# Kernel tuning notes

Measured on AMD Instinct MI355X. Metric: run time of the kernel, lower is better.

## Reference

```python
import jax, jax.numpy as jnp
import numpy as np

NUM_HEADS = 8

def setup_inputs() -> dict:
    key = jax.random.key(0)
    ks = jax.random.split(key, 7)
    B, S, H = 2, 4096, 512
    sc = 1.0 / np.sqrt(H)
    x = jax.random.normal(ks[0], (B, S, H), dtype=jnp.float32)
    Wq = jax.random.normal(ks[1], (H, H), dtype=jnp.float32) * sc
    bq = jnp.zeros((H,), dtype=jnp.float32)
    Wk = jax.random.normal(ks[2], (H, H), dtype=jnp.float32) * sc
    bk = jnp.zeros((H,), dtype=jnp.float32)
    Wv = jax.random.normal(ks[3], (H, H), dtype=jnp.float32) * sc
    bv = jnp.zeros((H,), dtype=jnp.float32)
    return {"x": x, "Wq": Wq, "bq": bq, "Wk": Wk, "bk": bk, "Wv": Wv, "bv": bv}

def reference(x, Wq, bq, Wk, bk, Wv, bv):
    B, S, H = x.shape
    hd = H // NUM_HEADS
    def split_heads(t):  # [B,S,H] -> [B,nh,S,hd]
        return t.reshape(B, S, NUM_HEADS, hd).transpose(0, 2, 1, 3)
    q = split_heads(x @ Wq + bq)
    k = split_heads(x @ Wk + bk)
    v = split_heads(x @ Wv + bv)
    scores = jnp.einsum('bhqd,bhkd->bhqk', q, k) / jnp.sqrt(jnp.float32(hd))
    attn = jax.nn.softmax(scores, axis=-1)  # dropout is identity at inference
    out = jnp.einsum('bhqk,bhkd->bhqd', attn, v)
    return out.transpose(0, 2, 1, 3).reshape(B, S, H)
```

## Files before the change

### kernel.cpp

```cpp
#include <hip/hip_runtime.h>
#include <hip/hip_bf16.h>

typedef __attribute__((ext_vector_type(8))) short short8;
typedef __attribute__((ext_vector_type(4))) float float4v;
typedef __attribute__((ext_vector_type(16))) float f32x16;

using bf16 = __hip_bfloat16;

#define QSCALE 0.18033688011112042f

__device__ inline float fexp2(float x) { return __builtin_amdgcn_exp2f(x); }

__device__ inline short f2bf(float f) {
  __hip_bfloat16 h = __float2bfloat16(f);
  short s;
  __builtin_memcpy(&s, &h, 2);
  return s;
}

__device__ inline float4v mfma16(short8 a, short8 b, float4v c) {
  return __builtin_amdgcn_mfma_f32_16x16x32_bf16(a, b, c, 0, 0, 0);
}
__device__ inline f32x16 mfma32(short8 a, short8 b, f32x16 c) {
  return __builtin_amdgcn_mfma_f32_32x32x16_bf16(a, b, c, 0, 0, 0);
}
__device__ inline unsigned pk2(float lo, float hi) {
  __hip_bfloat16 l = __float2bfloat16(lo), h = __float2bfloat16(hi);
  unsigned short ls, hs;
  __builtin_memcpy(&ls, &l, 2);
  __builtin_memcpy(&hs, &h, 2);
  return (unsigned)ls | ((unsigned)hs << 16);
}


__global__ __launch_bounds__(256) void conv_x_kernel(const float* __restrict__ x,
                                                     bf16* __restrict__ xb) {
  int i = blockIdx.x * 256 + threadIdx.x;
  const float4v* src = reinterpret_cast<const float4v*>(x);
  float4v a = src[(size_t)i * 2];
  float4v c = src[(size_t)i * 2 + 1];
  short8 o;
  o[0] = f2bf(a[0]); o[1] = f2bf(a[1]); o[2] = f2bf(a[2]); o[3] = f2bf(a[3]);
  o[4] = f2bf(c[0]); o[5] = f2bf(c[1]); o[6] = f2bf(c[2]); o[7] = f2bf(c[3]);
  *reinterpret_cast<short8*>(xb + (size_t)i * 8) = o;
}

__global__ void conv_w_kernel(const float* __restrict__ Wq, const float* __restrict__ Wk,
                              const float* __restrict__ Wv, bf16* __restrict__ wt) {
  __shared__ float tile[32][33];
  int z = blockIdx.z;
  const float* W = (z == 0) ? Wq : (z == 1) ? Wk : Wv;
  int n = blockIdx.x * 32 + threadIdx.x;
  int k = blockIdx.y * 32 + threadIdx.y;
  tile[threadIdx.y][threadIdx.x] = W[(size_t)k * 512 + n];
  __syncthreads();
  int nn = blockIdx.x * 32 + threadIdx.y;
  int kk = blockIdx.y * 32 + threadIdx.x;
  wt[(size_t)z * 512 * 512 + (size_t)nn * 512 + kk] = __float2bfloat16(tile[threadIdx.x][threadIdx.y]);
}


__global__ __launch_bounds__(256) void qkv_gemm_kernel(
    const bf16* __restrict__ xb, const bf16* __restrict__ wt,
    const float* __restrict__ bq, const float* __restrict__ bk, const float* __restrict__ bv,
    bf16* __restrict__ qb, bf16* __restrict__ kbuf, bf16* __restrict__ vt) {
  __shared__ bf16 Xs[64][72];
  __shared__ bf16 Ws[64][72];
  const int m0 = blockIdx.x * 64;
  const int n0 = blockIdx.y * 64;
  const int z  = blockIdx.z;
  const bf16* W = wt + (size_t)z * 512 * 512;
  const float* bias = (z == 0) ? bq : (z == 1) ? bk : bv;
  const int t = threadIdx.x;
  const int lane = t & 63, wv = t >> 6;
  const int row = t >> 3, col8 = (t & 7) * 8;
  const int lo = lane & 15, g8 = (lane >> 4) * 8;
  float4v acc[4] = {};
  for (int k0 = 0; k0 < 512; k0 += 64) {
    *reinterpret_cast<short8*>(&Xs[row][col8])      = *reinterpret_cast<const short8*>(&xb[(size_t)(m0 + row) * 512 + k0 + col8]);
    *reinterpret_cast<short8*>(&Xs[row + 32][col8]) = *reinterpret_cast<const short8*>(&xb[(size_t)(m0 + row + 32) * 512 + k0 + col8]);
    *reinterpret_cast<short8*>(&Ws[row][col8])      = *reinterpret_cast<const short8*>(&W[(size_t)(n0 + row) * 512 + k0 + col8]);
    *reinterpret_cast<short8*>(&Ws[row + 32][col8]) = *reinterpret_cast<const short8*>(&W[(size_t)(n0 + row + 32) * 512 + k0 + col8]);
    __syncthreads();
    short8 a0 = *reinterpret_cast<const short8*>(&Xs[wv * 16 + lo][g8]);
    short8 a1 = *reinterpret_cast<const short8*>(&Xs[wv * 16 + lo][32 + g8]);
#pragma unroll
    for (int nt = 0; nt < 4; ++nt) {
      short8 b0 = *reinterpret_cast<const short8*>(&Ws[nt * 16 + lo][g8]);
      short8 b1 = *reinterpret_cast<const short8*>(&Ws[nt * 16 + lo][32 + g8]);
      acc[nt] = mfma16(a0, b0, acc[nt]);
      acc[nt] = mfma16(a1, b1, acc[nt]);
    }
    __syncthreads();
  }
#pragma unroll
  for (int nt = 0; nt < 4; ++nt) {
    int ncol = n0 + nt * 16 + lo;
    float bias_v = bias[ncol];
    int h = ncol >> 6, d = ncol & 63;
#pragma unroll
    for (int r = 0; r < 4; ++r) {
      int mrow = m0 + wv * 16 + (lane >> 4) * 4 + r;
      int bb = mrow >> 12, s = mrow & 4095;
      float v = acc[nt][r] + bias_v;
      size_t base = (size_t)(bb * 8 + h) * 262144;
      if (z == 2) {
        size_t idx = (size_t)((d >> 5) * 256 + (s >> 4)) * 512 + (d & 31) * 8 + ((s >> 3) & 1) * 256 + (s & 7);
        vt[base + idx] = __float2bfloat16(v);
      } else {
        size_t idx = (size_t)((s >> 5) * 4 + (d >> 4)) * 512 + (s & 31) * 8 + ((d >> 3) & 1) * 256 + (d & 7);
        if (z == 0) qb[base + idx] = __float2bfloat16(v * QSCALE);
        else        kbuf[base + idx] = __float2bfloat16(v);
      }
    }
  }
}


__device__ __forceinline__ void load_tiles(const bf16* __restrict__ kb2, const bf16* __restrict__ vb2,
                                           int tl, short8 (&kf)[2][4], short8 (&vf)[2][4]) {
#pragma unroll
  for (int c = 0; c < 2; ++c)
#pragma unroll
    for (int ds = 0; ds < 4; ++ds)
      kf[c][ds] = *reinterpret_cast<const short8*>(kb2 + ((size_t)(tl * 2 + c) * 4 + ds) * 512);
#pragma unroll
  for (int dt = 0; dt < 2; ++dt)
#pragma unroll
    for (int gs = 0; gs < 4; ++gs)
      vf[dt][gs] = *reinterpret_cast<const short8*>(vb2 + (size_t)(dt * 256 + tl * 4 + gs) * 512);
}

__device__ __forceinline__ void attn_step(const short8 (&kf)[2][4], const short8 (&vf)[2][4],
                                          const short8 (&qf)[4], f32x16& ot0, f32x16& ot1,
                                          float& m_run, float& l_run, int half) {
  f32x16 p0 = {}, p1 = {};
#pragma unroll
  for (int ds = 0; ds < 4; ++ds) {
    p0 = mfma32(kf[0][ds], qf[ds], p0);
    p1 = mfma32(kf[1][ds], qf[ds], p1);
  }

  float ma = fmaxf(p0[0], p0[1]), mb = fmaxf(p0[2], p0[3]);
  float mc = fmaxf(p1[0], p1[1]), md = fmaxf(p1[2], p1[3]);
#pragma unroll
  for (int r = 4; r < 16; r += 4) {
    ma = fmaxf(ma, fmaxf(p0[r], p0[r + 1]));
    mb = fmaxf(mb, fmaxf(p0[r + 2], p0[r + 3]));
    mc = fmaxf(mc, fmaxf(p1[r], p1[r + 1]));
    md = fmaxf(md, fmaxf(p1[r + 2], p1[r + 3]));
  }
  float pmax = fmaxf(fmaxf(ma, mb), fmaxf(mc, md));
  pmax = fmaxf(pmax, __shfl_xor(pmax, 32));

  if (__any(pmax > m_run + 8.0f)) {
    float mnew = fmaxf(m_run, pmax);
    float sc = fexp2(m_run - mnew);
    m_run = mnew;
    l_run *= sc;
#pragma unroll
    for (int r = 0; r < 16; ++r) { ot0[r] *= sc; ot1[r] *= sc; }
  }

  float s0 = 0.f, s1 = 0.f, s2 = 0.f, s3 = 0.f;
#pragma unroll
  for (int r = 0; r < 16; r += 4) {
    p0[r]     = fexp2(p0[r]     - m_run); s0 += p0[r];
    p0[r + 1] = fexp2(p0[r + 1] - m_run); s1 += p0[r + 1];
    p0[r + 2] = fexp2(p0[r + 2] - m_run); s2 += p0[r + 2];
    p0[r + 3] = fexp2(p0[r + 3] - m_run); s3 += p0[r + 3];
  }
#pragma unroll
  for (int r = 0; r < 16; r += 4) {
    p1[r]     = fexp2(p1[r]     - m_run); s0 += p1[r];
    p1[r + 1] = fexp2(p1[r + 1] - m_run); s1 += p1[r + 1];
    p1[r + 2] = fexp2(p1[r + 2] - m_run); s2 += p1[r + 2];
    p1[r + 3] = fexp2(p1[r + 3] - m_run); s3 += p1[r + 3];
  }
  float ls = (s0 + s1) + (s2 + s3);
  ls += __shfl_xor(ls, 32);
  l_run += ls;

  unsigned pa[2][2][4];
#pragma unroll
  for (int c = 0; c < 2; ++c) {
    const f32x16& pc = c ? p1 : p0;
    unsigned w[4][2];
#pragma unroll
    for (int cq = 0; cq < 4; ++cq) {
      w[cq][0] = pk2(pc[4 * cq],     pc[4 * cq + 1]);
      w[cq][1] = pk2(pc[4 * cq + 2], pc[4 * cq + 3]);
    }
#pragma unroll
    for (int s = 0; s < 2; ++s)
#pragma unroll
      for (int x = 0; x < 2; ++x) {
        unsigned u = w[2 * s][x], v = w[2 * s + 1][x];
        unsigned pu = __shfl_xor(u, 32), pv = __shfl_xor(v, 32);
        pa[c][s][x]     = half ? pv : u;
        pa[c][s][2 + x] = half ? v  : pu;
      }
  }

#pragma unroll
  for (int c = 0; c < 2; ++c)
#pragma unroll
    for (int s = 0; s < 2; ++s) {
      short8 pb;
      __builtin_memcpy(&pb, pa[c][s], 16);
      ot0 = mfma32(vf[0][c * 2 + s], pb, ot0);
      ot1 = mfma32(vf[1][c * 2 + s], pb, ot1);
    }
}

__global__ __launch_bounds__(256, 2) void attn_kernel(
    const bf16* __restrict__ qbuf, const bf16* __restrict__ kbuf,
    const bf16* __restrict__ vtbuf, float* __restrict__ out) {
  int bid = blockIdx.x;
  int sw = (bid & 7) * 64 + (bid >> 3);
  int bh = sw >> 5, qt = sw & 31;
  const int bI = bh >> 3, hh = bh & 7;
  const int t = threadIdx.x;
  const int wid = t >> 6, lane = t & 63;
  const int l31 = lane & 31, half = lane >> 5;
  const int q0 = qt * 128 + wid * 32;

  const bf16* kb2 = kbuf + (size_t)bh * 262144 + lane * 8;
  const bf16* vb2 = vtbuf + (size_t)bh * 262144 + lane * 8;

  short8 qf[4];
#pragma unroll
  for (int ds = 0; ds < 4; ++ds)
    qf[ds] = *reinterpret_cast<const short8*>(qbuf + (size_t)bh * 262144 + (size_t)((q0 >> 5) * 4 + ds) * 512 + lane * 8);

  f32x16 ot0 = {}, ot1 = {};
  float m_run = -1e30f, l_run = 0.f;

  short8 kfA[2][4], vfA[2][4], kfB[2][4], vfB[2][4];
  load_tiles(kb2, vb2, 0, kfA, vfA);
  for (int it = 0; it < 64; it += 2) {
    load_tiles(kb2, vb2, it + 1, kfB, vfB);
    attn_step(kfA, vfA, qf, ot0, ot1, m_run, l_run, half);
    load_tiles(kb2, vb2, (it + 2) & 63, kfA, vfA);
    attn_step(kfB, vfB, qf, ot0, ot1, m_run, l_run, half);
  }

  float inv = 1.0f / l_run;
  int q = q0 + l31;
  float* obase = out + ((size_t)bI * 4096 + q) * 512 + hh * 64;
#pragma unroll
  for (int cq = 0; cq < 4; ++cq) {
    float4v o0, o1;
#pragma unroll
    for (int rr = 0; rr < 4; ++rr) {
      o0[rr] = ot0[4 * cq + rr] * inv;
      o1[rr] = ot1[4 * cq + rr] * inv;
    }
    *reinterpret_cast<float4v*>(obase + 8 * cq + 4 * half) = o0;
    *reinterpret_cast<float4v*>(obase + 32 + 8 * cq + 4 * half) = o1;
  }
}


extern "C" void kernel_launch(void* const* d_in, const int* in_sizes, int n_in,
                              void* d_out, int out_size, void* d_ws, size_t ws_size,
                              hipStream_t stream) {
  const float* x  = (const float*)d_in[0];
  const float* Wq = (const float*)d_in[1];
  const float* bq = (const float*)d_in[2];
  const float* Wk = (const float*)d_in[3];
  const float* bk = (const float*)d_in[4];
  const float* Wv = (const float*)d_in[5];
  const float* bv = (const float*)d_in[6];
  float* out = (float*)d_out;

  char* ws = (char*)d_ws;
  bf16* xb = (bf16*)(ws + 0);
  bf16* wt = (bf16*)(ws + 8388608);
  bf16* qb = (bf16*)(ws + 9961472);
  bf16* kb = (bf16*)(ws + 18350080);
  bf16* vt = (bf16*)(ws + 26738688);

  conv_x_kernel<<<2048, 256, 0, stream>>>(x, xb);
  conv_w_kernel<<<dim3(16, 16, 3), dim3(32, 32), 0, stream>>>(Wq, Wk, Wv, wt);
  qkv_gemm_kernel<<<dim3(128, 8, 3), 256, 0, stream>>>(xb, wt, bq, bk, bv, qb, kb, vt);
  attn_kernel<<<512, 256, 0, stream>>>(qb, kb, vt, out);
}
```

Baseline: 154.9 us.

## Process two query tiles per wave to reuse K/V fragments

Each wave now handles 64 query rows (two 32-row tiles) and reuses every loaded K/V tile fragment for both. This halves the number of blocks and the global K/V loads per query. In exchange, occupancy drops to one 256-thread block per CU with a 256-block grid, and register usage roughly doubles for accumulators and Q fragments. Latency hiding may suffer as a result.

```diff
diff --git a/kernel.cpp b/kernel.cpp
--- a/kernel.cpp
+++ b/kernel.cpp
@@ -213,51 +213,61 @@
     }
 }
 
-__global__ __launch_bounds__(256, 2) void attn_kernel(
+__global__ __launch_bounds__(256, 1) void attn_kernel(
     const bf16* __restrict__ qbuf, const bf16* __restrict__ kbuf,
     const bf16* __restrict__ vtbuf, float* __restrict__ out) {
   int bid = blockIdx.x;
-  int sw = (bid & 7) * 64 + (bid >> 3);
-  int bh = sw >> 5, qt = sw & 31;
+  int sw = (bid & 7) * 32 + (bid >> 3);
+  int bh = sw >> 4, qt = sw & 15;
   const int bI = bh >> 3, hh = bh & 7;
   const int t = threadIdx.x;
   const int wid = t >> 6, lane = t & 63;
   const int l31 = lane & 31, half = lane >> 5;
-  const int q0 = qt * 128 + wid * 32;
+  const int q0 = qt * 256 + wid * 64;
 
   const bf16* kb2 = kbuf + (size_t)bh * 262144 + lane * 8;
   const bf16* vb2 = vtbuf + (size_t)bh * 262144 + lane * 8;
 
-  short8 qf[4];
-#pragma unroll
-  for (int ds = 0; ds < 4; ++ds)
-    qf[ds] = *reinterpret_cast<const short8*>(qbuf + (size_t)bh * 262144 + (size_t)((q0 >> 5) * 4 + ds) * 512 + lane * 8);
-
-  f32x16 ot0 = {}, ot1 = {};
-  float m_run = -1e30f, l_run = 0.f;
+  short8 qf0[4], qf1[4];
+#pragma unroll
+  for (int ds = 0; ds < 4; ++ds) {
+    qf0[ds] = *reinterpret_cast<const short8*>(qbuf + (size_t)bh * 262144 + (size_t)(((q0 >> 5) + 0) * 4 + ds) * 512 + lane * 8);
+    qf1[ds] = *reinterpret_cast<const short8*>(qbuf + (size_t)bh * 262144 + (size_t)(((q0 >> 5) + 1) * 4 + ds) * 512 + lane * 8);
+  }
+
+  f32x16 oa0 = {}, oa1 = {}, ob0 = {}, ob1 = {};
+  float mA = -1e30f, lA = 0.f, mB = -1e30f, lB = 0.f;
 
   short8 kfA[2][4], vfA[2][4], kfB[2][4], vfB[2][4];
   load_tiles(kb2, vb2, 0, kfA, vfA);
   for (int it = 0; it < 64; it += 2) {
     load_tiles(kb2, vb2, it + 1, kfB, vfB);
-    attn_step(kfA, vfA, qf, ot0, ot1, m_run, l_run, half);
+    attn_step(kfA, vfA, qf0, oa0, oa1, mA, lA, half);
+    attn_step(kfA, vfA, qf1, ob0, ob1, mB, lB, half);
     load_tiles(kb2, vb2, (it + 2) & 63, kfA, vfA);
-    attn_step(kfB, vfB, qf, ot0, ot1, m_run, l_run, half);
-  }
-
-  float inv = 1.0f / l_run;
-  int q = q0 + l31;
-  float* obase = out + ((size_t)bI * 4096 + q) * 512 + hh * 64;
-#pragma unroll
-  for (int cq = 0; cq < 4; ++cq) {
-    float4v o0, o1;
-#pragma unroll
-    for (int rr = 0; rr < 4; ++rr) {
-      o0[rr] = ot0[4 * cq + rr] * inv;
-      o1[rr] = ot1[4 * cq + rr] * inv;
-    }
-    *reinterpret_cast<float4v*>(obase + 8 * cq + 4 * half) = o0;
-    *reinterpret_cast<float4v*>(obase + 32 + 8 * cq + 4 * half) = o1;
+    attn_step(kfB, vfB, qf0, oa0, oa1, mA, lA, half);
+    attn_step(kfB, vfB, qf1, ob0, ob1, mB, lB, half);
+  }
+
+  float invA = 1.0f / lA, invB = 1.0f / lB;
+#pragma unroll
+  for (int set = 0; set < 2; ++set) {
+    const f32x16& t0 = set ? ob0 : oa0;
+    const f32x16& t1 = set ? ob1 : oa1;
+    float inv = set ? invB : invA;
+    int q = q0 + set * 32 + l31;
+    float* obase = out + ((size_t)bI * 4096 + q) * 512 + hh * 64;
+#pragma unroll
+    for (int cq = 0; cq < 4; ++cq) {
+      float4v o0, o1;
+#pragma unroll
+      for (int rr = 0; rr < 4; ++rr) {
+        o0[rr] = t0[4 * cq + rr] * inv;
+        o1[rr] = t1[4 * cq + rr] * inv;
+      }
+      *reinterpret_cast<float4v*>(obase + 8 * cq + 4 * half) = o0;
+      *reinterpret_cast<float4v*>(obase + 32 + 8 * cq + 4 * half) = o1;
+    }
   }
 }
 
@@ -284,5 +294,5 @@
   conv_x_kernel<<<2048, 256, 0, stream>>>(x, xb);
   conv_w_kernel<<<dim3(16, 16, 3), dim3(32, 32), 0, stream>>>(Wq, Wk, Wv, wt);
   qkv_gemm_kernel<<<dim3(128, 8, 3), 256, 0, stream>>>(xb, wt, bq, bk, bv, qb, kb, vt);
-  attn_kernel<<<512, 256, 0, stream>>>(qb, kb, vt, out);
-}
+  attn_kernel<<<256, 256, 0, stream>>>(qb, kb, vt, out);
+}
```

Measured after the change: 161.8 us. +4.5%, slower.
